# Optimization experiments

Hardware: AMD Instinct MI355X
Metric: run time of the kernel (lower is better)

Reference implementation:

```python
import jax, jax.numpy as jnp
import numpy as np

N, E, G = 50000, 800000, 512
IN_C, H, EC, L, OUT_C = 16, 128, 16, 4, 1

def _lin(k, fi, fo):
    return jax.random.normal(k, (fi, fo), dtype=jnp.float32) / np.sqrt(fi)

def setup_inputs() -> dict:
    key = jax.random.key(0)
    ks = jax.random.split(key, 32)
    inp = {
        'x_nodes': jax.random.normal(ks[0], (N, IN_C), dtype=jnp.float32),
        'x_edges': jax.random.normal(ks[1], (E, EC), dtype=jnp.float32),
        'edge_index': jax.random.randint(ks[2], (2, E), 0, N),
        'batch': jnp.sort(jax.random.randint(ks[3], (N,), 0, G)),
    }
    # embed_nodes
    inp['emb_w1'] = _lin(ks[4], IN_C, H); inp['emb_b1'] = jnp.zeros((H,), jnp.float32)
    inp['emb_w2'] = _lin(ks[5], H, H);    inp['emb_b2'] = jnp.zeros((H,), jnp.float32)
    # per-layer edge_net / node_net weights, stacked over L
    kk = jax.random.split(ks[6], 4 * L)
    inp['ew1'] = jnp.stack([_lin(kk[i], 2 * H + EC, H) for i in range(L)])
    inp['eb1'] = jnp.zeros((L, H), jnp.float32)
    inp['ew2'] = jnp.stack([_lin(kk[L + i], H, H) for i in range(L)])
    inp['eb2'] = jnp.zeros((L, H), jnp.float32)
    inp['nw1'] = jnp.stack([_lin(kk[2 * L + i], 2 * H, H) for i in range(L)])
    inp['nb1'] = jnp.zeros((L, H), jnp.float32)
    inp['nw2'] = jnp.stack([_lin(kk[3 * L + i], H, H) for i in range(L)])
    inp['nb2'] = jnp.zeros((L, H), jnp.float32)
    # pre_readout / readout
    inp['pr_w1'] = _lin(ks[7], H, H); inp['pr_b1'] = jnp.zeros((H,), jnp.float32)
    inp['pr_w2'] = _lin(ks[8], H, H); inp['pr_b2'] = jnp.zeros((H,), jnp.float32)
    inp['ro_w1'] = _lin(ks[9], H, H); inp['ro_b1'] = jnp.zeros((H,), jnp.float32)
    inp['ro_w2'] = _lin(ks[10], H, OUT_C); inp['ro_b2'] = jnp.zeros((OUT_C,), jnp.float32)
    return inp

def _gnn_forward(x_nodes, x_edges, emb_w1, emb_b1, emb_w2, emb_b2,
                 ew1, eb1, ew2, eb2, nw1, nb1, nw2, nb2,
                 pr_w1, pr_b1, pr_w2, pr_b2, ro_w1, ro_b1, ro_w2, ro_b2,
                 edge_index, batch):
    silu = jax.nn.silu
    sender, receiver = edge_index[0], edge_index[1]
    # embed_nodes
    h = silu(x_nodes @ emb_w1 + emb_b1) @ emb_w2 + emb_b2  # [N, H]
    for l in range(L):
        state = jnp.concatenate((h[sender], h[receiver], x_edges), axis=1)  # [E, 2H+EC]
        msg = silu(silu(state @ ew1[l] + eb1[l]) @ ew2[l] + eb2[l])  # [E, H]
        aggr = jax.ops.segment_sum(msg, receiver, num_segments=N)  # [N, H]
        h = silu(jnp.concatenate((h, aggr), axis=1) @ nw1[l] + nb1[l]) @ nw2[l] + nb2[l]
    h = silu(h @ pr_w1 + pr_b1) @ pr_w2 + pr_b2
    pooled = jax.ops.segment_sum(h, batch, num_segments=G)  # [G, H]
    out = silu(pooled @ ro_w1 + ro_b1) @ ro_w2 + ro_b2  # [G, 1]
    return jnp.squeeze(out)

def reference(x_nodes, x_edges, edge_index, batch,
              emb_w1, emb_b1, emb_w2, emb_b2,
              ew1, eb1, ew2, eb2, nw1, nb1, nw2, nb2,
              pr_w1, pr_b1, pr_w2, pr_b2, ro_w1, ro_b1, ro_w2, ro_b2):
    return _gnn_forward(x_nodes, x_edges, emb_w1, emb_b1, emb_w2, emb_b2,
                        ew1, eb1, ew2, eb2, nw1, nb1, nw2, nb2,
                        pr_w1, pr_b1, pr_w2, pr_b2, ro_w1, ro_b1, ro_w2, ro_b2,
                        edge_index, batch)
```

## Files before the change

kernel.cpp:

```cpp
#include <hip/hip_runtime.h>


typedef short bf16x8 __attribute__((ext_vector_type(8)));
typedef float f32x4 __attribute__((ext_vector_type(4)));

union U8 { bf16x8 v; unsigned short u[8]; unsigned int d[4]; };

__device__ __forceinline__ float bf2f(unsigned short u) {
    union { unsigned int i; float f; } x; x.i = ((unsigned int)u) << 16; return x.f;
}
__device__ __forceinline__ float u32lo2f(unsigned int d) {
    union { unsigned int i; float f; } x; x.i = d << 16; return x.f;
}
__device__ __forceinline__ float u32hi2f(unsigned int d) {
    union { unsigned int i; float f; } x; x.i = d & 0xffff0000u; return x.f;
}
__device__ __forceinline__ unsigned short f2bf(float f) {
    union { float f; unsigned int i; } x; x.f = f;
    unsigned int r = x.i + 0x7FFFu + ((x.i >> 16) & 1u);
    return (unsigned short)(r >> 16);
}
__device__ __forceinline__ unsigned int cvt_pk_bf16(float lo, float hi) {
    unsigned int r;
    asm("v_cvt_pk_bf16_f32 %0, %1, %2" : "=v"(r) : "v"(lo), "v"(hi));
    return r;
}
__device__ __forceinline__ float siluf(float x) { return x / (1.0f + __expf(-x)); }
__device__ __forceinline__ float silu_fast(float x) {
    float e;
    asm("v_exp_f32 %0, %1" : "=v"(e) : "v"(x * -1.44269504089f));
    float r;
    asm("v_rcp_f32 %0, %1" : "=v"(r) : "v"(e + 1.0f));
    return x * r;
}

__global__ void k_hist(const int* __restrict__ recv, int* __restrict__ counts, int E) {
    int i = blockIdx.x * 256 + threadIdx.x;
    if (i < E) atomicAdd(&counts[recv[i]], 1);
}

__global__ __launch_bounds__(1024) void k_scan1(const int* __restrict__ counts,
                                                int* __restrict__ offsets,
                                                int* __restrict__ bsum, int n) {
    __shared__ int buf[1024];
    int i = blockIdx.x * 1024 + threadIdx.x;
    int v = (i < n) ? counts[i] : 0;
    buf[threadIdx.x] = v;
    __syncthreads();
    for (int off = 1; off < 1024; off <<= 1) {
        int t = 0;
        if ((int)threadIdx.x >= off) t = buf[threadIdx.x - off];
        __syncthreads();
        if ((int)threadIdx.x >= off) buf[threadIdx.x] += t;
        __syncthreads();
    }
    if (i < n) offsets[i] = buf[threadIdx.x] - v;
    if (threadIdx.x == 1023) bsum[blockIdx.x] = buf[1023];
}

__global__ void k_scan2(int* __restrict__ bsum, int nb) {
    if (threadIdx.x == 0 && blockIdx.x == 0) {
        int acc = 0;
        for (int b = 0; b < nb; ++b) { int v = bsum[b]; bsum[b] = acc; acc += v; }
    }
}

__global__ __launch_bounds__(1024) void k_scan3(int* __restrict__ offsets,
                                                const int* __restrict__ bsum,
                                                int n, int E) {
    int i = blockIdx.x * 1024 + threadIdx.x;
    if (i < n) offsets[i] += bsum[blockIdx.x];
    if (i == 0) offsets[n] = E;
}

__global__ void k_scatter(const int* __restrict__ send, const int* __restrict__ recv,
                          const int* __restrict__ offsets, int* __restrict__ cursor,
                          int* __restrict__ ss, int* __restrict__ sr,
                          int* __restrict__ perm, int E) {
    int i = blockIdx.x * 256 + threadIdx.x;
    if (i < E) {
        int r = recv[i];
        int pos = offsets[r] + atomicAdd(&cursor[r], 1);
        ss[pos] = send[i];
        sr[pos] = r;
        perm[pos] = i;
    }
}

__global__ void k_permute_xe(const float* __restrict__ xe, const int* __restrict__ perm,
                             unsigned short* __restrict__ out, int E) {
    int t = blockIdx.x * 256 + threadIdx.x;
    if (t < E * 4) {
        int pos = t >> 2, q = t & 3;
        int e = perm[pos];
        float4 v = *(const float4*)(xe + (size_t)e * 16 + q * 4);
        ushort4 o;
        o.x = f2bf(v.x); o.y = f2bf(v.y); o.z = f2bf(v.z); o.w = f2bf(v.w);
        *(ushort4*)(out + (size_t)pos * 16 + q * 4) = o;
    }
}

struct WJob { const float* src; unsigned short* dst; int rows; int perm; };
struct WJobs { WJob j[31]; };

__global__ __launch_bounds__(256) void k_wconv(WJobs jobs) {
    WJob jb = jobs.j[blockIdx.x];
    int n = jb.rows * 128;
    if (jb.perm) {
        for (int i = threadIdx.x; i < n; i += 256) {
            int c = i >> 7, slot = i & 127;
            int feat = (slot >> 3) + 16 * (slot & 7);
            jb.dst[c * 128 + slot] = f2bf(jb.src[feat * 128 + c]);
        }
    } else {
        for (int i = threadIdx.x; i < n; i += 256) {
            int k = i >> 7, c = i & 127;
            jb.dst[c * jb.rows + k] = f2bf(jb.src[i]);
        }
    }
}

__global__ __launch_bounds__(256) void k_embed1(const float* __restrict__ x,
                                                const float* __restrict__ w1,
                                                const float* __restrict__ b1,
                                                unsigned short* __restrict__ out, int N) {
    int idx = blockIdx.x * 256 + threadIdx.x;
    int n = idx >> 6, lane = idx & 63;
    if (n >= N) return;
    const float* xr = x + (size_t)n * 16;
    float xv[16];
#pragma unroll
    for (int k = 0; k < 16; k += 4) {
        float4 v = *(const float4*)(xr + k);
        xv[k] = v.x; xv[k + 1] = v.y; xv[k + 2] = v.z; xv[k + 3] = v.w;
    }
    int c0 = lane * 2;
    float a0 = b1[c0], a1 = b1[c0 + 1];
#pragma unroll
    for (int k = 0; k < 16; ++k) {
        float2 w = *(const float2*)(w1 + k * 128 + c0);
        a0 += xv[k] * w.x; a1 += xv[k] * w.y;
    }
    *(unsigned int*)(out + (size_t)n * 128 + c0) = cvt_pk_bf16(siluf(a0), siluf(a1));
}

__device__ __forceinline__ void load_frags(const unsigned short* __restrict__ A,
                                           int r0, int colb, int kg, int M,
                                           bf16x8 (&Af)[2][4]) {
#pragma unroll
    for (int rf = 0; rf < 2; ++rf) {
        int row = r0 + rf * 16 + colb;
        if (row < M) {
#pragma unroll
            for (int ks = 0; ks < 4; ++ks)
                Af[rf][ks] = *(const bf16x8*)(A + (size_t)row * 128 + ks * 32 + kg * 8);
        } else {
            U8 z;
#pragma unroll
            for (int i = 0; i < 8; ++i) z.u[i] = 0;
#pragma unroll
            for (int ks = 0; ks < 4; ++ks) Af[rf][ks] = z.v;
        }
    }
}

__device__ __forceinline__ void mma_block(const bf16x8 (&Af)[2][4],
                                          const unsigned short* sW,
                                          int colb, int kg, f32x4 (&C)[2][8]) {
#pragma unroll
    for (int ks = 0; ks < 4; ++ks) {
#pragma unroll
        for (int cf = 0; cf < 8; ++cf) {
            bf16x8 B = *(const bf16x8*)(sW + (colb + 16 * cf) * 136 + ks * 32 + kg * 8);
#pragma unroll
            for (int rf = 0; rf < 2; ++rf)
                C[rf][cf] = __builtin_amdgcn_mfma_f32_16x16x32_bf16(Af[rf][ks], B, C[rf][cf], 0, 0, 0);
        }
    }
}

#define WLOAD(WT) do { \
    _Pragma("unroll") \
    for (int k_ = 0; k_ < 8; ++k_) \
        wreg[k_] = *(const bf16x8*)((WT) + tid * 8 + k_ * 2048); \
} while (0)

#define WWRITE() do { __syncthreads(); \
    _Pragma("unroll") \
    for (int k_ = 0; k_ < 8; ++k_) { \
        int i_ = tid * 8 + k_ * 2048; \
        *(bf16x8*)(sW + (i_ >> 7) * 136 + (i_ & 127)) = wreg[k_]; \
    } \
    __syncthreads(); } while (0)

__global__ __launch_bounds__(256, 2) void k_node(
    const unsigned short* __restrict__ A1, const unsigned short* __restrict__ WT1,
    const unsigned short* __restrict__ A2, const unsigned short* __restrict__ WT2,
    const float* __restrict__ b12, int act1,
    unsigned short* __restrict__ out1,
    const unsigned short* __restrict__ WT3, const float* __restrict__ b3,
    unsigned short* __restrict__ out3,
    const unsigned short* __restrict__ WTs, const unsigned short* __restrict__ WTr,
    unsigned short* __restrict__ outPs, unsigned short* __restrict__ outPr,
    int M) {
    __shared__ unsigned short sW[128 * 136];
    __shared__ unsigned short sT[128 * 136];
    int tid = threadIdx.x, lane = tid & 63, w = tid >> 6;
    int r0 = blockIdx.x * 128 + w * 32;
    int colb = lane & 15, kg = lane >> 4;
    bf16x8 wreg[8];

    f32x4 C[2][8];
#pragma unroll
    for (int cf = 0; cf < 8; ++cf) {
        float bb = b12[colb + 16 * cf];
        C[0][cf] = (f32x4){bb, bb, bb, bb};
        C[1][cf] = C[0][cf];
    }
    bf16x8 Af[2][4], Af2[2][4];
    WLOAD(WT1);
    load_frags(A1, r0, colb, kg, M, Af);
    if (WT2) load_frags(A2, r0, colb, kg, M, Af2);
    WWRITE();
    if (WT2) WLOAD(WT2);
    mma_block(Af, sW, colb, kg, C);
    if (WT2) {
        WWRITE();
        if (WT3) WLOAD(WT3);
        mma_block(Af2, sW, colb, kg, C);
    } else if (WT3) {
        WLOAD(WT3);
    }
#pragma unroll
    for (int rf = 0; rf < 2; ++rf) {
#pragma unroll
        for (int cf = 0; cf < 8; ++cf) {
            int col = colb + 16 * cf;
#pragma unroll
            for (int j = 0; j < 4; ++j) {
                float v = C[rf][cf][j];
                if (act1) v = siluf(v);
                unsigned short bv = f2bf(v);
                int lrow = w * 32 + rf * 16 + kg * 4 + j;
                sT[lrow * 136 + col] = bv;
                if (out1) {
                    int row = r0 + rf * 16 + kg * 4 + j;
                    if (row < M) out1[(size_t)row * 128 + col] = bv;
                }
            }
        }
    }

    if (WT3) {
        WWRITE();
        if (WTs) WLOAD(WTs);
        bf16x8 At[2][4];
#pragma unroll
        for (int rf = 0; rf < 2; ++rf)
#pragma unroll
            for (int ks = 0; ks < 4; ++ks)
                At[rf][ks] = *(const bf16x8*)(sT + (w * 32 + rf * 16 + colb) * 136 + ks * 32 + kg * 8);
#pragma unroll
        for (int cf = 0; cf < 8; ++cf) {
            float bb = b3[colb + 16 * cf];
            C[0][cf] = (f32x4){bb, bb, bb, bb};
            C[1][cf] = C[0][cf];
        }
        mma_block(At, sW, colb, kg, C);
#pragma unroll
        for (int rf = 0; rf < 2; ++rf) {
#pragma unroll
            for (int cf = 0; cf < 8; ++cf) {
                int col = colb + 16 * cf;
#pragma unroll
                for (int j = 0; j < 4; ++j) {
                    unsigned short bv = f2bf(C[rf][cf][j]);
                    int row = r0 + rf * 16 + kg * 4 + j;
                    if (row < M) out3[(size_t)row * 128 + col] = bv;
                    if (WTs) sT[(w * 32 + rf * 16 + kg * 4 + j) * 136 + col] = bv;
                }
            }
        }
    } else if (WTs) {
        WLOAD(WTs);
    }

    if (WTs) {
        WWRITE();
        WLOAD(WTr);
        bf16x8 At[2][4];
#pragma unroll
        for (int rf = 0; rf < 2; ++rf)
#pragma unroll
            for (int ks = 0; ks < 4; ++ks)
                At[rf][ks] = *(const bf16x8*)(sT + (w * 32 + rf * 16 + colb) * 136 + ks * 32 + kg * 8);
#pragma unroll
        for (int rf = 0; rf < 2; ++rf)
#pragma unroll
            for (int cf = 0; cf < 8; ++cf) C[rf][cf] = (f32x4){0.f, 0.f, 0.f, 0.f};
        mma_block(At, sW, colb, kg, C);
#pragma unroll
        for (int rf = 0; rf < 2; ++rf) {
#pragma unroll
            for (int j = 0; j < 4; ++j) {
                int row = r0 + rf * 16 + kg * 4 + j;
                if (row < M) {
                    U8 o;
#pragma unroll
                    for (int q = 0; q < 4; ++q)
                        o.d[q] = cvt_pk_bf16(C[rf][2 * q][j], C[rf][2 * q + 1][j]);
                    *(bf16x8*)(outPs + (size_t)row * 128 + colb * 8) = o.v;
                }
            }
        }
        WWRITE();
#pragma unroll
        for (int rf = 0; rf < 2; ++rf)
#pragma unroll
            for (int cf = 0; cf < 8; ++cf) C[rf][cf] = (f32x4){0.f, 0.f, 0.f, 0.f};
        mma_block(At, sW, colb, kg, C);
#pragma unroll
        for (int rf = 0; rf < 2; ++rf) {
#pragma unroll
            for (int j = 0; j < 4; ++j) {
                int row = r0 + rf * 16 + kg * 4 + j;
                if (row < M) {
                    U8 o;
#pragma unroll
                    for (int q = 0; q < 4; ++q)
                        o.d[q] = cvt_pk_bf16(C[rf][2 * q][j], C[rf][2 * q + 1][j]);
                    *(bf16x8*)(outPr + (size_t)row * 128 + colb * 8) = o.v;
                }
            }
        }
    }
}

__global__ __launch_bounds__(256, 3) void k_msg(
    const unsigned short* __restrict__ Ps, const unsigned short* __restrict__ Pr,
    const unsigned short* __restrict__ xes,
    const int* __restrict__ ss, const int* __restrict__ sr,
    const unsigned short* __restrict__ WeT, const float* __restrict__ b1,
    const unsigned short* __restrict__ W2T, const float* __restrict__ b2,
    unsigned short* __restrict__ aggr, float* __restrict__ pbuf,
    int* __restrict__ pid, int ntiles) {
    __shared__ unsigned short sW2[128 * 136];
    __shared__ unsigned short sT[64 * 136];
    __shared__ float sB2[128];
    __shared__ int sRid[64];
    int tid = threadIdx.x, lane = tid & 63, w = tid >> 6;
    int colb = lane & 15, kg = lane >> 4;
    int R0 = w * 16, rb = R0 + kg * 4;

    for (int i = tid * 8; i < 16384; i += 2048)
        *(bf16x8*)(sW2 + (i >> 7) * 136 + (i & 127)) = *(const bf16x8*)(W2T + i);
    if (tid < 128) sB2[tid] = b2[tid];
    bf16x8 WeB[8];
#pragma unroll
    for (int cf = 0; cf < 8; ++cf) {
        if (kg < 2) WeB[cf] = *(const bf16x8*)(WeT + (colb + 16 * cf) * 16 + kg * 8);
        else { U8 z; for (int i = 0; i < 8; ++i) z.u[i] = 0; WeB[cf] = z.v; }
    }
    float b1v[8];
#pragma unroll
    for (int cf = 0; cf < 8; ++cf) b1v[cf] = b1[colb + 16 * cf];
    int s = lane * 2;
    int c0 = (s >> 3) + 16 * (s & 7);
    __syncthreads();

    int stride = gridDim.x;
    int t = blockIdx.x;
    U8 zz; for (int i = 0; i < 8; ++i) zz.u[i] = 0;
    bf16x8 Axe = zz.v;
    U8 gp[8];
    int4 s4 = *(const int4*)(ss + (t << 6) + rb);
    int4 r4 = *(const int4*)(sr + (t << 6) + rb);

#define ISSUE_GATHER(S4, R4, TT) do { \
        gp[0].v = *(const bf16x8*)(Ps + (size_t)(S4).x * 128 + colb * 8); \
        gp[1].v = *(const bf16x8*)(Ps + (size_t)(S4).y * 128 + colb * 8); \
        gp[2].v = *(const bf16x8*)(Ps + (size_t)(S4).z * 128 + colb * 8); \
        gp[3].v = *(const bf16x8*)(Ps + (size_t)(S4).w * 128 + colb * 8); \
        gp[4].v = *(const bf16x8*)(Pr + (size_t)(R4).x * 128 + colb * 8); \
        gp[5].v = *(const bf16x8*)(Pr + (size_t)(R4).y * 128 + colb * 8); \
        gp[6].v = *(const bf16x8*)(Pr + (size_t)(R4).z * 128 + colb * 8); \
        gp[7].v = *(const bf16x8*)(Pr + (size_t)(R4).w * 128 + colb * 8); \
        if (kg < 2) Axe = *(const bf16x8*)(xes + (size_t)(((TT) << 6) + R0 + colb) * 16 + kg * 8); \
    } while (0)

    ISSUE_GATHER(s4, r4, t);
    for (;;) {
        if (colb == 0) {
            sRid[rb] = r4.x; sRid[rb + 1] = r4.y; sRid[rb + 2] = r4.z; sRid[rb + 3] = r4.w;
        }
        int tn = t + stride;
        bool more = tn < ntiles;
        int4 s4n, r4n;
        if (more) {
            s4n = *(const int4*)(ss + (tn << 6) + rb);
            r4n = *(const int4*)(sr + (tn << 6) + rb);
        }
        f32x4 xc[8];
#pragma unroll
        for (int cf = 0; cf < 8; ++cf) {
            f32x4 bb = (f32x4){b1v[cf], b1v[cf], b1v[cf], b1v[cf]};
            xc[cf] = __builtin_amdgcn_mfma_f32_16x16x32_bf16(Axe, WeB[cf], bb, 0, 0, 0);
        }
#pragma unroll
        for (int j = 0; j < 4; ++j) {
            U8 o;
#pragma unroll
            for (int q = 0; q < 4; ++q) {
                float v0 = u32lo2f(gp[j].d[q]) + u32lo2f(gp[4 + j].d[q]) + xc[2 * q][j];
                float v1 = u32hi2f(gp[j].d[q]) + u32hi2f(gp[4 + j].d[q]) + xc[2 * q + 1][j];
                o.d[q] = cvt_pk_bf16(silu_fast(v0), silu_fast(v1));
            }
            *(bf16x8*)(sT + (rb + j) * 136 + colb * 8) = o.v;
        }
        int tcur = t;
        if (more) ISSUE_GATHER(s4n, r4n, tn);
        asm volatile("s_waitcnt lgkmcnt(0)" ::: "memory");
        __builtin_amdgcn_sched_barrier(0);
        bf16x8 Bt[4];
#pragma unroll
        for (int ks = 0; ks < 4; ++ks)
            Bt[ks] = *(const bf16x8*)(sT + (R0 + colb) * 136 + ks * 32 + kg * 8);
        f32x4 m[8];
#pragma unroll
        for (int acf = 0; acf < 8; ++acf)
            m[acf] = *(const f32x4*)(sB2 + acf * 16 + kg * 4);
#pragma unroll
        for (int ks = 0; ks < 4; ++ks) {
#pragma unroll
            for (int acf = 0; acf < 8; ++acf) {
                bf16x8 Aw = *(const bf16x8*)(sW2 + (16 * acf + colb) * 136 + ks * 32 + kg * 8);
                m[acf] = __builtin_amdgcn_mfma_f32_16x16x32_bf16(Aw, Bt[ks], m[acf], 0, 0, 0);
            }
        }
#pragma unroll
        for (int j = 0; j < 4; ++j) {
            U8 o;
#pragma unroll
            for (int q = 0; q < 4; ++q)
                o.d[q] = cvt_pk_bf16(silu_fast(m[2 * q][j]), silu_fast(m[2 * q + 1][j]));
            *(bf16x8*)(sT + (R0 + colb) * 136 + (kg * 4 + j) * 8) = o.v;
        }
        asm volatile("s_waitcnt lgkmcnt(0)" ::: "memory");
        __builtin_amdgcn_sched_barrier(0);
        {
            int run = tcur * 4 + w;
            float a0 = 0.f, a1 = 0.f;
            int prev = sRid[R0];
            bool first = true;
            for (int i = 0; i < 16; ++i) {
                int rid = sRid[R0 + i];
                if (rid != prev) {
                    if (first) {
                        float2 vv; vv.x = a0; vv.y = a1;
                        *(float2*)(pbuf + (size_t)(2 * run) * 128 + s) = vv;
                        if (lane == 0) pid[2 * run] = prev;
                        first = false;
                    } else {
                        aggr[(size_t)prev * 128 + c0] = f2bf(a0);
                        aggr[(size_t)prev * 128 + c0 + 16] = f2bf(a1);
                    }
                    a0 = 0.f; a1 = 0.f; prev = rid;
                }
                unsigned int v = *(const unsigned int*)(sT + (R0 + i) * 136 + s);
                a0 += u32lo2f(v); a1 += u32hi2f(v);
            }
            float2 vv; vv.x = a0; vv.y = a1;
            if (first) {
                *(float2*)(pbuf + (size_t)(2 * run) * 128 + s) = vv;
                if (lane == 0) { pid[2 * run] = prev; pid[2 * run + 1] = -1; }
            } else {
                *(float2*)(pbuf + (size_t)(2 * run + 1) * 128 + s) = vv;
                if (lane == 0) pid[2 * run + 1] = prev;
            }
        }
        if (!more) break;
        s4 = s4n; r4 = r4n; t = tn;
    }
#undef ISSUE_GATHER
}

__global__ __launch_bounds__(256) void k_fix(
    const float* __restrict__ pbuf, const int* __restrict__ pid,
    const int* __restrict__ offsets, unsigned short* __restrict__ aggr, int N) {
    int gw = (blockIdx.x * 256 + threadIdx.x) >> 6;
    int lane = threadIdx.x & 63;
    int nw = (gridDim.x * 256) >> 6;
    int s = lane * 2;
    int c0 = (s >> 3) + 16 * (s & 7);
    for (int n = gw; n < N; n += nw) {
        int o0 = offsets[n], o1 = offsets[n + 1];
        if (o0 >= o1) continue;
        int t0 = o0 >> 4, t1 = (o1 - 1) >> 4;
        if (t0 == t1 && o0 > (t0 << 4) && o1 <= (t0 << 4) + 15) continue;
        float a0 = 0.f, a1 = 0.f;
        for (int tt = t0; tt <= t1; ++tt) {
            if (pid[2 * tt] == n) {
                float2 v = *(const float2*)(pbuf + (size_t)(2 * tt) * 128 + s);
                a0 += v.x; a1 += v.y;
            }
            if (pid[2 * tt + 1] == n) {
                float2 v = *(const float2*)(pbuf + (size_t)(2 * tt + 1) * 128 + s);
                a0 += v.x; a1 += v.y;
            }
        }
        aggr[(size_t)n * 128 + c0] = f2bf(a0);
        aggr[(size_t)n * 128 + c0 + 16] = f2bf(a1);
    }
}

__device__ __forceinline__ int lowerb(const int* a, int n, int v) {
    int lo = 0, hi = n;
    while (lo < hi) { int mid = (lo + hi) >> 1; if (a[mid] < v) lo = mid + 1; else hi = mid; }
    return lo;
}

__global__ __launch_bounds__(128) void k_pool(const unsigned short* __restrict__ hpr,
                                              const int* __restrict__ batch,
                                              float* __restrict__ pooled, int N) {
    __shared__ int s_lo, s_hi;
    int g = blockIdx.x;
    if (threadIdx.x == 0) { s_lo = lowerb(batch, N, g); s_hi = lowerb(batch, N, g + 1); }
    __syncthreads();
    int c = threadIdx.x;
    float acc = 0.f;
    for (int r = s_lo; r < s_hi; ++r) acc += bf2f(hpr[(size_t)r * 128 + c]);
    pooled[(size_t)g * 128 + c] = acc;
}

__global__ __launch_bounds__(128) void k_readout(const float* __restrict__ pooled,
                                                 const float* __restrict__ w1,
                                                 const float* __restrict__ b1,
                                                 const float* __restrict__ w2,
                                                 const float* __restrict__ b2,
                                                 float* __restrict__ out) {
    __shared__ float sp[128];
    __shared__ float sred[2];
    int g = blockIdx.x, t = threadIdx.x;
    sp[t] = pooled[(size_t)g * 128 + t];
    __syncthreads();
    float acc = b1[t];
    for (int k = 0; k < 128; ++k) acc += sp[k] * w1[k * 128 + t];
    float val = siluf(acc) * w2[t];
#pragma unroll
    for (int off = 32; off; off >>= 1) val += __shfl_down(val, off);
    if ((t & 63) == 0) sred[t >> 6] = val;
    __syncthreads();
    if (t == 0) out[g] = sred[0] + sred[1] + b2[0];
}

extern "C" void kernel_launch(void* const* d_in, const int* in_sizes, int n_in,
                              void* d_out, int out_size, void* d_ws, size_t ws_size,
                              hipStream_t stream) {
    const float* x_nodes = (const float*)d_in[0];
    const float* x_edges = (const float*)d_in[1];
    const int* edge_index = (const int*)d_in[2];
    const int* batch = (const int*)d_in[3];
    const float* emb_w1 = (const float*)d_in[4];
    const float* emb_b1 = (const float*)d_in[5];
    const float* emb_w2 = (const float*)d_in[6];
    const float* emb_b2 = (const float*)d_in[7];
    const float* ew1 = (const float*)d_in[8];
    const float* eb1 = (const float*)d_in[9];
    const float* ew2 = (const float*)d_in[10];
    const float* eb2 = (const float*)d_in[11];
    const float* nw1 = (const float*)d_in[12];
    const float* nb1 = (const float*)d_in[13];
    const float* nw2 = (const float*)d_in[14];
    const float* nb2 = (const float*)d_in[15];
    const float* pr_w1 = (const float*)d_in[16];
    const float* pr_b1 = (const float*)d_in[17];
    const float* pr_w2 = (const float*)d_in[18];
    const float* pr_b2 = (const float*)d_in[19];
    const float* ro_w1 = (const float*)d_in[20];
    const float* ro_b1 = (const float*)d_in[21];
    const float* ro_w2 = (const float*)d_in[22];
    const float* ro_b2 = (const float*)d_in[23];

    const int N = in_sizes[0] / 16;
    const int E = in_sizes[1] / 16;
    const int G = 512;
    const int L = 4;
    const int nruns = E >> 4;
    const int ntiles = E >> 6;

    char* p = (char*)d_ws;
    auto alloc = [&](size_t bytes) {
        void* r = p;
        p += (bytes + 255) & ~(size_t)255;
        return r;
    };
    int* counts = (int*)alloc((size_t)N * 4);
    int* cursor = (int*)alloc((size_t)N * 4);
    int* offsets = (int*)alloc((size_t)(N + 1) * 4);
    int* bsum = (int*)alloc((size_t)256 * 4);
    int* ss = (int*)alloc((size_t)E * 4);
    int* sr = (int*)alloc((size_t)E * 4);
    int* perm = (int*)alloc((size_t)E * 4);
    unsigned short* xes = (unsigned short*)alloc((size_t)E * 16 * 2);
    unsigned short* h = (unsigned short*)alloc((size_t)N * 128 * 2);
    unsigned short* t0buf = (unsigned short*)alloc((size_t)N * 128 * 2);
    unsigned short* Ps = (unsigned short*)alloc((size_t)N * 128 * 2);
    unsigned short* Pr = (unsigned short*)alloc((size_t)N * 128 * 2);
    unsigned short* aggr = (unsigned short*)alloc((size_t)N * 128 * 2);
    unsigned short* hpr = (unsigned short*)alloc((size_t)N * 128 * 2);
    float* pooled = (float*)alloc((size_t)G * 128 * 4);
    float* pbuf = (float*)alloc((size_t)nruns * 2 * 128 * 4);
    int* pid = (int*)alloc((size_t)nruns * 2 * 4);

    const size_t WSZ = 128 * 128;
    unsigned short* wt_emb2 = (unsigned short*)alloc(WSZ * 2);
    unsigned short *wtWs[4], *wtWr[4], *wtWe[4], *wtW2[4], *wtN1a[4], *wtN1b[4], *wtN2[4];
    for (int l = 0; l < L; ++l) {
        wtWs[l] = (unsigned short*)alloc(WSZ * 2);
        wtWr[l] = (unsigned short*)alloc(WSZ * 2);
        wtWe[l] = (unsigned short*)alloc((size_t)16 * 128 * 2);
        wtW2[l] = (unsigned short*)alloc(WSZ * 2);
        wtN1a[l] = (unsigned short*)alloc(WSZ * 2);
        wtN1b[l] = (unsigned short*)alloc(WSZ * 2);
        wtN2[l] = (unsigned short*)alloc(WSZ * 2);
    }
    unsigned short* wt_pr1 = (unsigned short*)alloc(WSZ * 2);
    unsigned short* wt_pr2 = (unsigned short*)alloc(WSZ * 2);

    const int* send = edge_index;
    const int* recv = edge_index + E;

    hipMemsetAsync(counts, 0, (size_t)N * 4, stream);
    hipMemsetAsync(cursor, 0, (size_t)N * 4, stream);
    hipMemsetAsync(aggr, 0, (size_t)N * 128 * 2, stream);
    k_hist<<<(E + 255) / 256, 256, 0, stream>>>(recv, counts, E);
    int nb = (N + 1023) / 1024;
    k_scan1<<<nb, 1024, 0, stream>>>(counts, offsets, bsum, N);
    k_scan2<<<1, 64, 0, stream>>>(bsum, nb);
    k_scan3<<<nb, 1024, 0, stream>>>(offsets, bsum, N, E);
    k_scatter<<<(E + 255) / 256, 256, 0, stream>>>(send, recv, offsets, cursor, ss, sr, perm, E);
    k_permute_xe<<<(E * 4 + 255) / 256, 256, 0, stream>>>(x_edges, perm, xes, E);

    WJobs jobs;
    int nj = 0;
    auto addj = [&](const float* s, unsigned short* d, int rows, int pm) {
        jobs.j[nj].src = s; jobs.j[nj].dst = d; jobs.j[nj].rows = rows; jobs.j[nj].perm = pm; ++nj;
    };
    addj(emb_w2, wt_emb2, 128, 0);
    for (int l = 0; l < L; ++l) {
        const float* ew1_l = ew1 + (size_t)l * 272 * 128;
        addj(ew1_l, wtWs[l], 128, 0);
        addj(ew1_l + 128 * 128, wtWr[l], 128, 0);
        addj(ew1_l + 256 * 128, wtWe[l], 16, 0);
        addj(ew2 + (size_t)l * WSZ, wtW2[l], 128, 1);
        const float* nw1_l = nw1 + (size_t)l * 256 * 128;
        addj(nw1_l, wtN1a[l], 128, 0);
        addj(nw1_l + 128 * 128, wtN1b[l], 128, 0);
        addj(nw2 + (size_t)l * WSZ, wtN2[l], 128, 0);
    }
    addj(pr_w1, wt_pr1, 128, 0);
    addj(pr_w2, wt_pr2, 128, 0);
    k_wconv<<<nj, 256, 0, stream>>>(jobs);

    int gb = (N + 127) / 128;
    k_embed1<<<(N * 64 + 255) / 256, 256, 0, stream>>>(x_nodes, emb_w1, emb_b1, t0buf, N);
    k_node<<<gb, 256, 0, stream>>>(t0buf, wt_emb2, nullptr, nullptr, emb_b2, 0,
                                   h, nullptr, nullptr, nullptr,
                                   wtWs[0], wtWr[0], Ps, Pr, N);

    int mg = ntiles < 2048 ? ntiles : 2048;
    for (int l = 0; l < L; ++l) {
        k_msg<<<mg, 256, 0, stream>>>(Ps, Pr, xes, ss, sr, wtWe[l], eb1 + l * 128,
                                      wtW2[l], eb2 + l * 128, aggr, pbuf, pid, ntiles);
        k_fix<<<2048, 256, 0, stream>>>(pbuf, pid, offsets, aggr, N);
        k_node<<<gb, 256, 0, stream>>>(h, wtN1a[l], aggr, wtN1b[l], nb1 + l * 128, 1,
                                       nullptr, wtN2[l], nb2 + l * 128, h,
                                       (l < L - 1) ? wtWs[l + 1] : nullptr,
                                       (l < L - 1) ? wtWr[l + 1] : nullptr,
                                       Ps, Pr, N);
    }

    k_node<<<gb, 256, 0, stream>>>(h, wt_pr1, nullptr, nullptr, pr_b1, 1,
                                   nullptr, wt_pr2, pr_b2, hpr,
                                   nullptr, nullptr, nullptr, nullptr, N);
    k_pool<<<G, 128, 0, stream>>>(hpr, batch, pooled, N);
    k_readout<<<G, 128, 0, stream>>>(pooled, ro_w1, ro_b1, ro_w2, ro_b2, (float*)d_out);
}
```

Measured before the change: 885.9 us.

## Use 512-thread message blocks with per-wave independent 16-edge runs

Each wave of the message kernel now walks its own sequence of 16-edge runs instead of the whole block sharing a 64-edge tile. The block grows to 512 threads (8 waves), so the 128x128 edge-MLP weight matrix in shared memory is loaded once for more waves. The grid is capped at 1024 blocks with launch bounds (512,2). The intent is to spread the weight staging and LDS cost over more waves and let waves progress independently. The cost is more shared memory per block and tighter register limits, which could lower occupancy or cause register spills.

Measured after the change: 877.1 us, median of 2. No clear change (-1.0%).

```diff
diff --git a/kernel.cpp b/kernel.cpp
--- a/kernel.cpp
+++ b/kernel.cpp
@@ -336,23 +336,23 @@
     }
 }
 
-__global__ __launch_bounds__(256, 3) void k_msg(
+__global__ __launch_bounds__(512, 2) void k_msg(
     const unsigned short* __restrict__ Ps, const unsigned short* __restrict__ Pr,
     const unsigned short* __restrict__ xes,
     const int* __restrict__ ss, const int* __restrict__ sr,
     const unsigned short* __restrict__ WeT, const float* __restrict__ b1,
     const unsigned short* __restrict__ W2T, const float* __restrict__ b2,
     unsigned short* __restrict__ aggr, float* __restrict__ pbuf,
-    int* __restrict__ pid, int ntiles) {
+    int* __restrict__ pid, int nruns) {
     __shared__ unsigned short sW2[128 * 136];
-    __shared__ unsigned short sT[64 * 136];
+    __shared__ unsigned short sT[128 * 136];
     __shared__ float sB2[128];
-    __shared__ int sRid[64];
+    __shared__ int sRid[128];
     int tid = threadIdx.x, lane = tid & 63, w = tid >> 6;
     int colb = lane & 15, kg = lane >> 4;
-    int R0 = w * 16, rb = R0 + kg * 4;
-
-    for (int i = tid * 8; i < 16384; i += 2048)
+    int R0 = w * 16, rb4 = kg * 4;
+
+    for (int i = tid * 8; i < 16384; i += 4096)
         *(bf16x8*)(sW2 + (i >> 7) * 136 + (i & 127)) = *(const bf16x8*)(W2T + i);
     if (tid < 128) sB2[tid] = b2[tid];
     bf16x8 WeB[8];
@@ -368,15 +368,16 @@
     int c0 = (s >> 3) + 16 * (s & 7);
     __syncthreads();
 
-    int stride = gridDim.x;
-    int t = blockIdx.x;
+    int stride = gridDim.x * 8;
+    int run = blockIdx.x * 8 + w;
+    if (run >= nruns) return;
     U8 zz; for (int i = 0; i < 8; ++i) zz.u[i] = 0;
     bf16x8 Axe = zz.v;
     U8 gp[8];
-    int4 s4 = *(const int4*)(ss + (t << 6) + rb);
-    int4 r4 = *(const int4*)(sr + (t << 6) + rb);
-
-#define ISSUE_GATHER(S4, R4, TT) do { \
+    int4 s4 = *(const int4*)(ss + (run << 4) + rb4);
+    int4 r4 = *(const int4*)(sr + (run << 4) + rb4);
+
+#define ISSUE_GATHER(S4, R4, RR) do { \
         gp[0].v = *(const bf16x8*)(Ps + (size_t)(S4).x * 128 + colb * 8); \
         gp[1].v = *(const bf16x8*)(Ps + (size_t)(S4).y * 128 + colb * 8); \
         gp[2].v = *(const bf16x8*)(Ps + (size_t)(S4).z * 128 + colb * 8); \
@@ -385,20 +386,21 @@
         gp[5].v = *(const bf16x8*)(Pr + (size_t)(R4).y * 128 + colb * 8); \
         gp[6].v = *(const bf16x8*)(Pr + (size_t)(R4).z * 128 + colb * 8); \
         gp[7].v = *(const bf16x8*)(Pr + (size_t)(R4).w * 128 + colb * 8); \
-        if (kg < 2) Axe = *(const bf16x8*)(xes + (size_t)(((TT) << 6) + R0 + colb) * 16 + kg * 8); \
+        if (kg < 2) Axe = *(const bf16x8*)(xes + (size_t)(((RR) << 4) + colb) * 16 + kg * 8); \
     } while (0)
 
-    ISSUE_GATHER(s4, r4, t);
+    ISSUE_GATHER(s4, r4, run);
     for (;;) {
         if (colb == 0) {
-            sRid[rb] = r4.x; sRid[rb + 1] = r4.y; sRid[rb + 2] = r4.z; sRid[rb + 3] = r4.w;
-        }
-        int tn = t + stride;
-        bool more = tn < ntiles;
+            sRid[R0 + rb4] = r4.x; sRid[R0 + rb4 + 1] = r4.y;
+            sRid[R0 + rb4 + 2] = r4.z; sRid[R0 + rb4 + 3] = r4.w;
+        }
+        int rn = run + stride;
+        bool more = rn < nruns;
         int4 s4n, r4n;
         if (more) {
-            s4n = *(const int4*)(ss + (tn << 6) + rb);
-            r4n = *(const int4*)(sr + (tn << 6) + rb);
+            s4n = *(const int4*)(ss + (rn << 4) + rb4);
+            r4n = *(const int4*)(sr + (rn << 4) + rb4);
         }
         f32x4 xc[8];
 #pragma unroll
@@ -415,10 +417,10 @@
                 float v1 = u32hi2f(gp[j].d[q]) + u32hi2f(gp[4 + j].d[q]) + xc[2 * q + 1][j];
                 o.d[q] = cvt_pk_bf16(silu_fast(v0), silu_fast(v1));
             }
-            *(bf16x8*)(sT + (rb + j) * 136 + colb * 8) = o.v;
-        }
-        int tcur = t;
-        if (more) ISSUE_GATHER(s4n, r4n, tn);
+            *(bf16x8*)(sT + (R0 + rb4 + j) * 136 + colb * 8) = o.v;
+        }
+        int rcur = run;
+        if (more) ISSUE_GATHER(s4n, r4n, rn);
         asm volatile("s_waitcnt lgkmcnt(0)" ::: "memory");
         __builtin_amdgcn_sched_barrier(0);
         bf16x8 Bt[4];
@@ -448,7 +450,6 @@
         asm volatile("s_waitcnt lgkmcnt(0)" ::: "memory");
         __builtin_amdgcn_sched_barrier(0);
         {
-            int run = tcur * 4 + w;
             float a0 = 0.f, a1 = 0.f;
             int prev = sRid[R0];
             bool first = true;
@@ -457,8 +458,8 @@
                 if (rid != prev) {
                     if (first) {
                         float2 vv; vv.x = a0; vv.y = a1;
-                        *(float2*)(pbuf + (size_t)(2 * run) * 128 + s) = vv;
-                        if (lane == 0) pid[2 * run] = prev;
+                        *(float2*)(pbuf + (size_t)(2 * rcur) * 128 + s) = vv;
+                        if (lane == 0) pid[2 * rcur] = prev;
                         first = false;
                     } else {
                         aggr[(size_t)prev * 128 + c0] = f2bf(a0);
@@ -471,15 +472,15 @@
             }
             float2 vv; vv.x = a0; vv.y = a1;
             if (first) {
-                *(float2*)(pbuf + (size_t)(2 * run) * 128 + s) = vv;
-                if (lane == 0) { pid[2 * run] = prev; pid[2 * run + 1] = -1; }
+                *(float2*)(pbuf + (size_t)(2 * rcur) * 128 + s) = vv;
+                if (lane == 0) { pid[2 * rcur] = prev; pid[2 * rcur + 1] = -1; }
             } else {
-                *(float2*)(pbuf + (size_t)(2 * run + 1) * 128 + s) = vv;
-                if (lane == 0) pid[2 * run + 1] = prev;
+                *(float2*)(pbuf + (size_t)(2 * rcur + 1) * 128 + s) = vv;
+                if (lane == 0) pid[2 * rcur + 1] = prev;
             }
         }
         if (!more) break;
-        s4 = s4n; r4 = r4n; t = tn;
+        s4 = s4n; r4 = r4n; run = rn;
     }
 #undef ISSUE_GATHER
 }
@@ -586,7 +587,6 @@
     const int G = 512;
     const int L = 4;
     const int nruns = E >> 4;
-    const int ntiles = E >> 6;
 
     char* p = (char*)d_ws;
     auto alloc = [&](size_t bytes) {
@@ -668,10 +668,11 @@
                                    h, nullptr, nullptr, nullptr,
                                    wtWs[0], wtWr[0], Ps, Pr, N);
 
-    int mg = ntiles < 2048 ? ntiles : 2048;
+    int mg = (nruns + 7) / 8;
+    if (mg > 1024) mg = 1024;
     for (int l = 0; l < L; ++l) {
-        k_msg<<<mg, 256, 0, stream>>>(Ps, Pr, xes, ss, sr, wtWe[l], eb1 + l * 128,
-                                      wtW2[l], eb2 + l * 128, aggr, pbuf, pid, ntiles);
+        k_msg<<<mg, 512, 0, stream>>>(Ps, Pr, xes, ss, sr, wtWe[l], eb1 + l * 128,
+                                      wtW2[l], eb2 + l * 128, aggr, pbuf, pid, nruns);
         k_fix<<<2048, 256, 0, stream>>>(pbuf, pid, offsets, aggr, N);
         k_node<<<gb, 256, 0, stream>>>(h, wtN1a[l], aggr, wtN1b[l], nb1 + l * 128, 1,
                                        nullptr, wtN2[l], nb2 + l * 128, h,
```
